# Performance work log

Measured on AMD Instinct MI355X. Metric: run time of the kernel, lower is better.

Reference implementation:

```python
import jax, jax.numpy as jnp
import numpy as np

N, IN_DIM, HID, LAT, E = 8192, 512, 256, 128, 262144


def gcn_conv(x, W, b, src, dst, n):
    # PyG-style GCNConv: linear transform, add self-loops, D^-1/2 A D^-1/2 aggregation, bias.
    h = x @ W                                                  # [n, out]
    loops = jnp.arange(n)
    s = jnp.concatenate([src, loops])
    d = jnp.concatenate([dst, loops])
    deg = jax.ops.segment_sum(jnp.ones(s.shape[0], x.dtype), d, num_segments=n)
    dinv = jnp.where(deg > 0, jax.lax.rsqrt(deg), jnp.zeros((), x.dtype))
    norm = dinv[s] * dinv[d]                                   # [E+n]
    out = jax.ops.segment_sum(h[s] * norm[:, None], d, num_segments=n)
    return out + b


def setup_inputs() -> dict:
    key = jax.random.key(0)
    ks = jax.random.split(key, 9)
    x = jax.random.normal(ks[0], (N, IN_DIM), dtype=jnp.float32)
    edge_index = jax.random.randint(ks[1], (2, E), 0, N, dtype=jnp.int64)
    eps = jax.random.normal(ks[2], (N, LAT), dtype=jnp.float32)
    # Glorot-ish scaled params
    W1 = jax.random.normal(ks[3], (IN_DIM, HID), dtype=jnp.float32) / np.sqrt(IN_DIM)
    b1 = jnp.zeros((HID,), jnp.float32)
    Wmu = jax.random.normal(ks[4], (HID, LAT), dtype=jnp.float32) / np.sqrt(HID)
    bmu = jnp.zeros((LAT,), jnp.float32)
    Wls = jax.random.normal(ks[5], (HID, LAT), dtype=jnp.float32) / np.sqrt(HID)
    bls = jnp.zeros((LAT,), jnp.float32)
    return {"x": x, "edge_index": edge_index, "eps": eps,
            "W1": W1, "b1": b1, "Wmu": Wmu, "bmu": bmu, "Wls": Wls, "bls": bls}


def reference(x, edge_index, eps, W1, b1, Wmu, bmu, Wls, bls):
    src, dst = edge_index[0], edge_index[1]
    n = x.shape[0]
    h = jax.nn.relu(gcn_conv(x, W1, b1, src, dst, n))          # [N, HID]
    mu = gcn_conv(h, Wmu, bmu, src, dst, n)                    # [N, LAT]
    logstd = gcn_conv(h, Wls, bls, src, dst, n)                # [N, LAT]
    z = eps * jnp.exp(logstd) + mu                             # reparametrize (training mode)
    adj_recon = jax.nn.sigmoid(z @ z.T)                        # [N, N]
    return adj_recon, mu, logstd
```

## Files before the change

kernel.cpp:

```cpp
#include <hip/hip_runtime.h>

#define N_NODES 8192
#define IN_DIM  512
#define HID     256
#define LAT     128
#define NEDGE   262144

typedef __attribute__((ext_vector_type(8))) short  bf16x8;
typedef __attribute__((ext_vector_type(4))) float  f32x4;
typedef unsigned short u16;
typedef __attribute__((ext_vector_type(4))) unsigned short u16x4;

static __device__ inline u16 f2bf(float f) {
    unsigned u = __float_as_uint(f);
    unsigned r = (u + 0x7fffu + ((u >> 16) & 1u)) >> 16;
    return (u16)r;
}
static __device__ inline float bf2f(u16 s) {
    return __uint_as_float(((unsigned)s) << 16);
}

#define PREP_BLOCKS 5888

static __device__ inline void convw_body(const float* __restrict__ W,
                                         u16* __restrict__ th,
                                         u16* __restrict__ tl,
                                         int K, int N, int Kld, int roff, int e) {
    if (e >= K * N) return;
    int k = e / N, n = e - k * N;
    float f = W[e];
    u16 hi = f2bf(f);
    u16 lo = f2bf(f - bf2f(hi));
    size_t o = (size_t)(roff + n) * Kld + k;
    th[o] = hi;
    tl[o] = lo;
}

__global__ __launch_bounds__(256) void prep_kernel(const int* __restrict__ dst,
                                                   int* __restrict__ cnt,
                                                   const float* __restrict__ X,
                                                   u16* __restrict__ xh,
                                                   u16* __restrict__ xl,
                                                   const float* __restrict__ W1,
                                                   u16* __restrict__ w1h,
                                                   u16* __restrict__ w1l,
                                                   const float* __restrict__ Wmu,
                                                   const float* __restrict__ Wls,
                                                   u16* __restrict__ wch,
                                                   u16* __restrict__ wcl) {
    const int b = blockIdx.x, t = threadIdx.x;
    if (b < 1024) {
        int e = b * 256 + t;
        atomicAdd(&cnt[dst[e]], 1);
    } else if (b < 5120) {
        int idx = (b - 1024) * 256 + t;
        f32x4 v = *(const f32x4*)(X + (size_t)idx * 4);
        u16x4 h, l;
#pragma unroll
        for (int j = 0; j < 4; ++j) {
            h[j] = f2bf(v[j]);
            l[j] = f2bf(v[j] - bf2f(h[j]));
        }
        *(u16x4*)(xh + (size_t)idx * 4) = h;
        *(u16x4*)(xl + (size_t)idx * 4) = l;
    } else if (b < 5632) {
        convw_body(W1, w1h, w1l, IN_DIM, HID, IN_DIM, 0, (b - 5120) * 256 + t);
    } else if (b < 5760) {
        convw_body(Wmu, wch, wcl, HID, LAT, HID, 0, (b - 5632) * 256 + t);
    } else {
        convw_body(Wls, wch, wcl, HID, LAT, HID, LAT, (b - 5760) * 256 + t);
    }
}

__global__ __launch_bounds__(256) void scan_kernel(const int* __restrict__ cnt,
                                                   int* __restrict__ rowptr,
                                                   int* __restrict__ cursor,
                                                   float* __restrict__ dinv) {
    __shared__ int part[256];
    const int t = threadIdx.x;
    const int base = t * 32;
    int local[32];
    int s = 0;
#pragma unroll
    for (int i = 0; i < 32; ++i) {
        int cv = cnt[base + i];
        local[i] = s; s += cv;
        dinv[base + i] = rsqrtf((float)cv + 1.0f);
    }
    part[t] = s;
    __syncthreads();
    for (int off = 1; off < 256; off <<= 1) {
        int v = 0;
        if (t >= off) v = part[t - off];
        __syncthreads();
        if (t >= off) part[t] += v;
        __syncthreads();
    }
    int pre = (t == 0) ? 0 : part[t - 1];
#pragma unroll
    for (int i = 0; i < 32; ++i) {
        int r = pre + local[i];
        rowptr[base + i] = r;
        cursor[base + i] = r;
    }
    if (t == 255) rowptr[8192] = part[255];
}

static __device__ inline void gemm_body(const u16* __restrict__ Ah,
                                        const u16* __restrict__ Al,
                                        const u16* __restrict__ Bth,
                                        const u16* __restrict__ Btl,
                                        float* __restrict__ C,
                                        int K, int ldc, int bx, int by, int tid) {
    const int lane = tid & 63;
    const int wave = tid >> 6;
    const int l16 = lane & 15, quad = lane >> 4;
    const int rowBase = by * 128 + (wave >> 1) * 64;
    const int colBase = bx * 128 + (wave & 1) * 64;

    f32x4 acc[4][4] = {};

    for (int k0 = 0; k0 < K; k0 += 32) {
        const int kk = k0 + quad * 8;
        bf16x8 ah[4], al[4], bh[4], bl[4];
#pragma unroll
        for (int r = 0; r < 4; ++r) {
            int row = rowBase + r * 16 + l16;
            ah[r] = *(const bf16x8*)(Ah + (size_t)row * K + kk);
            al[r] = *(const bf16x8*)(Al + (size_t)row * K + kk);
        }
#pragma unroll
        for (int c = 0; c < 4; ++c) {
            int row = colBase + c * 16 + l16;
            bh[c] = *(const bf16x8*)(Bth + (size_t)row * K + kk);
            bl[c] = *(const bf16x8*)(Btl + (size_t)row * K + kk);
        }
#pragma unroll
        for (int r = 0; r < 4; ++r)
#pragma unroll
            for (int c = 0; c < 4; ++c) {
                acc[r][c] = __builtin_amdgcn_mfma_f32_16x16x32_bf16(ah[r], bh[c], acc[r][c], 0, 0, 0);
                acc[r][c] = __builtin_amdgcn_mfma_f32_16x16x32_bf16(ah[r], bl[c], acc[r][c], 0, 0, 0);
                acc[r][c] = __builtin_amdgcn_mfma_f32_16x16x32_bf16(al[r], bh[c], acc[r][c], 0, 0, 0);
            }
    }

#pragma unroll
    for (int r = 0; r < 4; ++r)
#pragma unroll
        for (int c = 0; c < 4; ++c)
#pragma unroll
            for (int i = 0; i < 4; ++i) {
                int orow = rowBase + r * 16 + quad * 4 + i;
                int ocol = colBase + c * 16 + l16;
                C[(size_t)orow * ldc + ocol] = acc[r][c][i];
            }
}

__global__ __launch_bounds__(256) void fillgemm_kernel(const u16* __restrict__ xh,
                                                       const u16* __restrict__ xl,
                                                       const u16* __restrict__ w1h,
                                                       const u16* __restrict__ w1l,
                                                       float* __restrict__ pre1,
                                                       const int* __restrict__ src,
                                                       const int* __restrict__ dst,
                                                       int* __restrict__ cursor,
                                                       int* __restrict__ ebuf) {
    const int b = blockIdx.x;
    if (b < 128) {
        gemm_body(xh, xl, w1h, w1l, pre1, IN_DIM, HID, b & 1, b >> 1, threadIdx.x);
    } else {
        int e = (b - 128) * 256 + threadIdx.x;
        int pos = atomicAdd(&cursor[dst[e]], 1);
        ebuf[pos] = src[e];
    }
}

__global__ __launch_bounds__(256) void gemm2_kernel(const u16* __restrict__ h1h,
                                                    const u16* __restrict__ h1l,
                                                    const u16* __restrict__ wch,
                                                    const u16* __restrict__ wcl,
                                                    float* __restrict__ pre2) {
    gemm_body(h1h, h1l, wch, wcl, pre2, HID, HID, blockIdx.x & 1, blockIdx.x >> 1, threadIdx.x);
}

__global__ __launch_bounds__(256) void gather1_kernel(const float* __restrict__ pre1,
                                                      u16* __restrict__ h1h,
                                                      u16* __restrict__ h1l,
                                                      const int* __restrict__ rowptr,
                                                      const int* __restrict__ ebuf,
                                                      const float* __restrict__ dinv,
                                                      const float* __restrict__ b1) {
    const int wave = threadIdx.x >> 6, lane = threadIdx.x & 63;
    const int v = blockIdx.x * 4 + wave;
    const int c = lane * 4;
    const float dv = dinv[v];
    f32x4 acc = *(const f32x4*)(pre1 + (size_t)v * HID + c);
    acc *= dv * dv;
    int i = rowptr[v], end = rowptr[v + 1];
    for (; i + 1 < end; i += 2) {
        int s0 = ebuf[i], s1 = ebuf[i + 1];
        float n0 = dv * dinv[s0], n1 = dv * dinv[s1];
        f32x4 h0 = *(const f32x4*)(pre1 + (size_t)s0 * HID + c);
        f32x4 h1v = *(const f32x4*)(pre1 + (size_t)s1 * HID + c);
#pragma unroll
        for (int j = 0; j < 4; ++j) acc[j] += n0 * h0[j] + n1 * h1v[j];
    }
    if (i < end) {
        int s0 = ebuf[i];
        float n0 = dv * dinv[s0];
        f32x4 h0 = *(const f32x4*)(pre1 + (size_t)s0 * HID + c);
#pragma unroll
        for (int j = 0; j < 4; ++j) acc[j] += n0 * h0[j];
    }
    f32x4 bb = *(const f32x4*)(b1 + c);
    u16x4 hv, lv;
#pragma unroll
    for (int j = 0; j < 4; ++j) {
        float h = fmaxf(acc[j] + bb[j], 0.0f);
        hv[j] = f2bf(h);
        lv[j] = f2bf(h - bf2f(hv[j]));
    }
    *(u16x4*)(h1h + (size_t)v * HID + c) = hv;
    *(u16x4*)(h1l + (size_t)v * HID + c) = lv;
}

__global__ __launch_bounds__(256) void gather2_kernel(const float* __restrict__ pre2,
                                                      const int* __restrict__ rowptr,
                                                      const int* __restrict__ ebuf,
                                                      const float* __restrict__ dinv,
                                                      const float* __restrict__ bmu,
                                                      const float* __restrict__ bls,
                                                      const float* __restrict__ eps,
                                                      float* __restrict__ out_mu,
                                                      float* __restrict__ out_ls,
                                                      u16* __restrict__ zhi,
                                                      u16* __restrict__ zlo) {
    const int wave = threadIdx.x >> 6, lane = threadIdx.x & 63;
    const int v = blockIdx.x * 4 + wave;
    const int c = lane * 4;
    const float dv = dinv[v];
    f32x4 acc = *(const f32x4*)(pre2 + (size_t)v * HID + c);
    acc *= dv * dv;
    int i = rowptr[v], end = rowptr[v + 1];
    for (; i + 1 < end; i += 2) {
        int s0 = ebuf[i], s1 = ebuf[i + 1];
        float n0 = dv * dinv[s0], n1 = dv * dinv[s1];
        f32x4 h0 = *(const f32x4*)(pre2 + (size_t)s0 * HID + c);
        f32x4 h1v = *(const f32x4*)(pre2 + (size_t)s1 * HID + c);
#pragma unroll
        for (int j = 0; j < 4; ++j) acc[j] += n0 * h0[j] + n1 * h1v[j];
    }
    if (i < end) {
        int s0 = ebuf[i];
        float n0 = dv * dinv[s0];
        f32x4 h0 = *(const f32x4*)(pre2 + (size_t)s0 * HID + c);
#pragma unroll
        for (int j = 0; j < 4; ++j) acc[j] += n0 * h0[j];
    }
    const float* bias = (lane < 32) ? (bmu + c) : (bls + (c - 128));
    f32x4 bb = *(const f32x4*)bias;
#pragma unroll
    for (int j = 0; j < 4; ++j) acc[j] += bb[j];

    f32x4 other;
#pragma unroll
    for (int j = 0; j < 4; ++j) other[j] = __shfl(acc[j], (lane + 32) & 63, 64);

    if (lane < 32) {
        int idx = v * LAT + c;
        f32x4 ep = *(const f32x4*)(eps + idx);
        __builtin_nontemporal_store(acc, (f32x4*)(out_mu + idx));
        u16x4 hv, lv;
#pragma unroll
        for (int j = 0; j < 4; ++j) {
            float z = ep[j] * __expf(other[j]) + acc[j];
            u16 hi = f2bf(z);
            hv[j] = hi;
            lv[j] = f2bf(z - bf2f(hi));
        }
        *(u16x4*)(zhi + idx) = hv;
        *(u16x4*)(zlo + idx) = lv;
    } else {
        int idx = v * LAT + (c - 128);
        __builtin_nontemporal_store(acc, (f32x4*)(out_ls + idx));
    }
}

#define NTRI 2080
__global__ __launch_bounds__(256) void zzt_kernel(const u16* __restrict__ zhi,
                                                  const u16* __restrict__ zlo,
                                                  float* __restrict__ out) {
    __shared__ float lds[4][16][68];
    const int lane = threadIdx.x & 63;
    const int wave = threadIdx.x >> 6;
    const int l16 = lane & 15, quad = lane >> 4;

    int bid = (blockIdx.x & 7) * 260 + (blockIdx.x >> 3);
    int by = (int)((sqrtf(8.0f * (float)bid + 1.0f) - 1.0f) * 0.5f);
    while ((by + 1) * (by + 2) / 2 <= bid) ++by;
    while (by * (by + 1) / 2 > bid) --by;
    const int bx = bid - by * (by + 1) / 2;

    const int rowBase = by * 128 + (wave >> 1) * 64;
    const int colBase = bx * 128 + (wave & 1) * 64;

    f32x4 acc[4][4] = {};

#pragma unroll
    for (int k0 = 0; k0 < LAT; k0 += 32) {
        const int kk = k0 + quad * 8;
        bf16x8 ah[4], al[4], bh[4], bl[4];
#pragma unroll
        for (int r = 0; r < 4; ++r) {
            int row = rowBase + r * 16 + l16;
            ah[r] = *(const bf16x8*)(zhi + (size_t)row * LAT + kk);
            al[r] = *(const bf16x8*)(zlo + (size_t)row * LAT + kk);
        }
#pragma unroll
        for (int c = 0; c < 4; ++c) {
            int row = colBase + c * 16 + l16;
            bh[c] = *(const bf16x8*)(zhi + (size_t)row * LAT + kk);
            bl[c] = *(const bf16x8*)(zlo + (size_t)row * LAT + kk);
        }
#pragma unroll
        for (int r = 0; r < 4; ++r)
#pragma unroll
            for (int c = 0; c < 4; ++c) {
                acc[r][c] = __builtin_amdgcn_mfma_f32_16x16x32_bf16(ah[r], bh[c], acc[r][c], 0, 0, 0);
                acc[r][c] = __builtin_amdgcn_mfma_f32_16x16x32_bf16(ah[r], bl[c], acc[r][c], 0, 0, 0);
                acc[r][c] = __builtin_amdgcn_mfma_f32_16x16x32_bf16(al[r], bh[c], acc[r][c], 0, 0, 0);
            }
    }

#pragma unroll
    for (int r = 0; r < 4; ++r)
#pragma unroll
        for (int c = 0; c < 4; ++c)
#pragma unroll
            for (int i = 0; i < 4; ++i)
                acc[r][c][i] = 1.0f / (1.0f + __expf(-acc[r][c][i]));

#pragma unroll
    for (int r = 0; r < 4; ++r) {
#pragma unroll
        for (int c = 0; c < 4; ++c)
#pragma unroll
            for (int i = 0; i < 4; ++i)
                lds[wave][quad * 4 + i][c * 16 + l16] = acc[r][c][i];
#pragma unroll
        for (int it = 0; it < 4; ++it) {
            f32x4 v = *(const f32x4*)&lds[wave][it * 4 + quad][l16 * 4];
            int orow = rowBase + r * 16 + it * 4 + quad;
            __builtin_nontemporal_store(v, (f32x4*)(out + (size_t)orow * N_NODES + colBase + l16 * 4));
        }
    }

    if (by != bx) {
#pragma unroll
        for (int c = 0; c < 4; ++c) {
#pragma unroll
            for (int r = 0; r < 4; ++r) {
                f32x4 tv = acc[r][c];
                *(f32x4*)&lds[wave][l16][r * 16 + quad * 4] = tv;
            }
#pragma unroll
            for (int it = 0; it < 4; ++it) {
                f32x4 v = *(const f32x4*)&lds[wave][it * 4 + quad][l16 * 4];
                int orow = colBase + c * 16 + it * 4 + quad;
                __builtin_nontemporal_store(v, (f32x4*)(out + (size_t)orow * N_NODES + rowBase + l16 * 4));
            }
        }
    }
}

extern "C" void kernel_launch(void* const* d_in, const int* in_sizes, int n_in,
                              void* d_out, int out_size, void* d_ws, size_t ws_size,
                              hipStream_t stream) {
    const float* x   = (const float*)d_in[0];
    const int*   ei  = (const int*)d_in[1];
    const float* eps = (const float*)d_in[2];
    const float* W1  = (const float*)d_in[3];
    const float* b1  = (const float*)d_in[4];
    const float* Wmu = (const float*)d_in[5];
    const float* bmu = (const float*)d_in[6];
    const float* Wls = (const float*)d_in[7];
    const float* bls = (const float*)d_in[8];
    const int* src = ei;
    const int* dst = ei + NEDGE;

    float* out = (float*)d_out;
    float* pre1 = out;
    float* pre2 = out + 2097152;
    int*   ibase  = (int*)(out + 4194304);
    int*   cnt    = ibase;
    int*   rowptr = ibase + 8192;
    int*   cursor = ibase + 16385;
    int*   ebuf   = ibase + 24577;
    u16* xhi    = (u16*)(out + 4587520);
    u16* xlo    = (u16*)(out + 6684672);
    u16* h1hi   = (u16*)(out + 8781824);
    u16* h1lo   = (u16*)(out + 9830400);
    u16* w1thi  = (u16*)(out + 10878976);
    u16* w1tlo  = (u16*)(out + 11010048);
    u16* wcathi = (u16*)(out + 11141120);
    u16* wcatlo = (u16*)(out + 11173888);
    float* out_mu = out + 67108864;
    float* out_ls = out + 68157440;

    float* dinv = (float*)d_ws;
    u16* zhi = (u16*)((char*)d_ws + 32768);
    u16* zlo = (u16*)((char*)d_ws + 32768 + 2097152);

    hipMemsetAsync(cnt, 0, 8192 * sizeof(int), stream);

    prep_kernel<<<PREP_BLOCKS, 256, 0, stream>>>(dst, cnt, x, xhi, xlo,
                                                 W1, w1thi, w1tlo, Wmu, Wls, wcathi, wcatlo);

    scan_kernel<<<1, 256, 0, stream>>>(cnt, rowptr, cursor, dinv);

    fillgemm_kernel<<<128 + 1024, 256, 0, stream>>>(xhi, xlo, w1thi, w1tlo, pre1,
                                                    src, dst, cursor, ebuf);

    gather1_kernel<<<N_NODES / 4, 256, 0, stream>>>(pre1, h1hi, h1lo, rowptr, ebuf, dinv, b1);

    gemm2_kernel<<<128, 256, 0, stream>>>(h1hi, h1lo, wcathi, wcatlo, pre2);

    gather2_kernel<<<N_NODES / 4, 256, 0, stream>>>(pre2, rowptr, ebuf, dinv, bmu, bls, eps,
                                                    out_mu, out_ls, zhi, zlo);

    zzt_kernel<<<NTRI, 256, 0, stream>>>(zhi, zlo, out);
}
```

Before: 495.5 us.

## Switch zzt to 32x32x16 MFMA and unroll gathers by four edges

The z·zᵀ kernel now uses 32x32x16 bf16 MFMA tiles (2x2 per wave) instead of 16x16x32 (4x4). Operands are swapped so that row-contiguous accumulator values can be staged through a larger LDS buffer for the direct and transposed stores. Both gather kernels add a 4-edge unrolled loop so more independent neighbor loads are in flight. The aim is to cut operand load instructions in the GEMM and raise memory-level parallelism in the gathers, at the cost of more LDS use and a more complex store remap.

```diff
diff --git a/kernel.cpp b/kernel.cpp
--- a/kernel.cpp
+++ b/kernel.cpp
@@ -6,8 +6,9 @@
 #define LAT     128
 #define NEDGE   262144
 
-typedef __attribute__((ext_vector_type(8))) short  bf16x8;
-typedef __attribute__((ext_vector_type(4))) float  f32x4;
+typedef __attribute__((ext_vector_type(8)))  short  bf16x8;
+typedef __attribute__((ext_vector_type(4)))  float  f32x4;
+typedef __attribute__((ext_vector_type(16))) float  f32x16;
 typedef unsigned short u16;
 typedef __attribute__((ext_vector_type(4))) unsigned short u16x4;
 
@@ -198,6 +199,18 @@
     f32x4 acc = *(const f32x4*)(pre1 + (size_t)v * HID + c);
     acc *= dv * dv;
     int i = rowptr[v], end = rowptr[v + 1];
+    for (; i + 3 < end; i += 4) {
+        int s0 = ebuf[i], s1 = ebuf[i + 1], s2 = ebuf[i + 2], s3 = ebuf[i + 3];
+        float n0 = dv * dinv[s0], n1 = dv * dinv[s1];
+        float n2 = dv * dinv[s2], n3 = dv * dinv[s3];
+        f32x4 h0 = *(const f32x4*)(pre1 + (size_t)s0 * HID + c);
+        f32x4 h1v = *(const f32x4*)(pre1 + (size_t)s1 * HID + c);
+        f32x4 h2 = *(const f32x4*)(pre1 + (size_t)s2 * HID + c);
+        f32x4 h3 = *(const f32x4*)(pre1 + (size_t)s3 * HID + c);
+#pragma unroll
+        for (int j = 0; j < 4; ++j)
+            acc[j] += (n0 * h0[j] + n1 * h1v[j]) + (n2 * h2[j] + n3 * h3[j]);
+    }
     for (; i + 1 < end; i += 2) {
         int s0 = ebuf[i], s1 = ebuf[i + 1];
         float n0 = dv * dinv[s0], n1 = dv * dinv[s1];
@@ -243,6 +256,18 @@
     f32x4 acc = *(const f32x4*)(pre2 + (size_t)v * HID + c);
     acc *= dv * dv;
     int i = rowptr[v], end = rowptr[v + 1];
+    for (; i + 3 < end; i += 4) {
+        int s0 = ebuf[i], s1 = ebuf[i + 1], s2 = ebuf[i + 2], s3 = ebuf[i + 3];
+        float n0 = dv * dinv[s0], n1 = dv * dinv[s1];
+        float n2 = dv * dinv[s2], n3 = dv * dinv[s3];
+        f32x4 h0 = *(const f32x4*)(pre2 + (size_t)s0 * HID + c);
+        f32x4 h1v = *(const f32x4*)(pre2 + (size_t)s1 * HID + c);
+        f32x4 h2 = *(const f32x4*)(pre2 + (size_t)s2 * HID + c);
+        f32x4 h3 = *(const f32x4*)(pre2 + (size_t)s3 * HID + c);
+#pragma unroll
+        for (int j = 0; j < 4; ++j)
+            acc[j] += (n0 * h0[j] + n1 * h1v[j]) + (n2 * h2[j] + n3 * h3[j]);
+    }
     for (; i + 1 < end; i += 2) {
         int s0 = ebuf[i], s1 = ebuf[i + 1];
         float n0 = dv * dinv[s0], n1 = dv * dinv[s1];
@@ -291,10 +316,11 @@
 __global__ __launch_bounds__(256) void zzt_kernel(const u16* __restrict__ zhi,
                                                   const u16* __restrict__ zlo,
                                                   float* __restrict__ out) {
-    __shared__ float lds[4][16][68];
+    __shared__ float lds[4][32][68];
     const int lane = threadIdx.x & 63;
     const int wave = threadIdx.x >> 6;
     const int l16 = lane & 15, quad = lane >> 4;
+    const int l32 = lane & 31, half = lane >> 5;
 
     int bid = (blockIdx.x & 7) * 260 + (blockIdx.x >> 3);
     int by = (int)((sqrtf(8.0f * (float)bid + 1.0f) - 1.0f) * 0.5f);
@@ -305,69 +331,74 @@
     const int rowBase = by * 128 + (wave >> 1) * 64;
     const int colBase = bx * 128 + (wave & 1) * 64;
 
-    f32x4 acc[4][4] = {};
-
-#pragma unroll
-    for (int k0 = 0; k0 < LAT; k0 += 32) {
-        const int kk = k0 + quad * 8;
-        bf16x8 ah[4], al[4], bh[4], bl[4];
-#pragma unroll
-        for (int r = 0; r < 4; ++r) {
-            int row = rowBase + r * 16 + l16;
-            ah[r] = *(const bf16x8*)(zhi + (size_t)row * LAT + kk);
-            al[r] = *(const bf16x8*)(zlo + (size_t)row * LAT + kk);
-        }
-#pragma unroll
-        for (int c = 0; c < 4; ++c) {
-            int row = colBase + c * 16 + l16;
-            bh[c] = *(const bf16x8*)(zhi + (size_t)row * LAT + kk);
-            bl[c] = *(const bf16x8*)(zlo + (size_t)row * LAT + kk);
-        }
-#pragma unroll
-        for (int r = 0; r < 4; ++r)
-#pragma unroll
-            for (int c = 0; c < 4; ++c) {
-                acc[r][c] = __builtin_amdgcn_mfma_f32_16x16x32_bf16(ah[r], bh[c], acc[r][c], 0, 0, 0);
-                acc[r][c] = __builtin_amdgcn_mfma_f32_16x16x32_bf16(ah[r], bl[c], acc[r][c], 0, 0, 0);
-                acc[r][c] = __builtin_amdgcn_mfma_f32_16x16x32_bf16(al[r], bh[c], acc[r][c], 0, 0, 0);
+    f32x16 acc[2][2] = {};
+
+#pragma unroll
+    for (int k = 0; k < 8; ++k) {
+        const int kk = k * 16 + half * 8;
+        bf16x8 xh[2], xl[2], yh[2], yl[2];
+#pragma unroll
+        for (int r = 0; r < 2; ++r) {
+            int row = rowBase + r * 32 + l32;
+            xh[r] = *(const bf16x8*)(zhi + (size_t)row * LAT + kk);
+            xl[r] = *(const bf16x8*)(zlo + (size_t)row * LAT + kk);
+        }
+#pragma unroll
+        for (int cc = 0; cc < 2; ++cc) {
+            int row = colBase + cc * 32 + l32;
+            yh[cc] = *(const bf16x8*)(zhi + (size_t)row * LAT + kk);
+            yl[cc] = *(const bf16x8*)(zlo + (size_t)row * LAT + kk);
+        }
+#pragma unroll
+        for (int r = 0; r < 2; ++r)
+#pragma unroll
+            for (int cc = 0; cc < 2; ++cc) {
+                acc[r][cc] = __builtin_amdgcn_mfma_f32_32x32x16_bf16(yh[cc], xh[r], acc[r][cc], 0, 0, 0);
+                acc[r][cc] = __builtin_amdgcn_mfma_f32_32x32x16_bf16(yh[cc], xl[r], acc[r][cc], 0, 0, 0);
+                acc[r][cc] = __builtin_amdgcn_mfma_f32_32x32x16_bf16(yl[cc], xh[r], acc[r][cc], 0, 0, 0);
             }
     }
 
 #pragma unroll
-    for (int r = 0; r < 4; ++r)
-#pragma unroll
-        for (int c = 0; c < 4; ++c)
-#pragma unroll
-            for (int i = 0; i < 4; ++i)
-                acc[r][c][i] = 1.0f / (1.0f + __expf(-acc[r][c][i]));
-
-#pragma unroll
-    for (int r = 0; r < 4; ++r) {
-#pragma unroll
-        for (int c = 0; c < 4; ++c)
-#pragma unroll
-            for (int i = 0; i < 4; ++i)
-                lds[wave][quad * 4 + i][c * 16 + l16] = acc[r][c][i];
-#pragma unroll
-        for (int it = 0; it < 4; ++it) {
+    for (int r = 0; r < 2; ++r)
+#pragma unroll
+        for (int cc = 0; cc < 2; ++cc)
+#pragma unroll
+            for (int i = 0; i < 16; ++i)
+                acc[r][cc][i] = 1.0f / (1.0f + __expf(-acc[r][cc][i]));
+
+#pragma unroll
+    for (int r = 0; r < 2; ++r) {
+#pragma unroll
+        for (int cc = 0; cc < 2; ++cc)
+#pragma unroll
+            for (int q = 0; q < 4; ++q) {
+                f32x4 v = { acc[r][cc][q * 4 + 0], acc[r][cc][q * 4 + 1],
+                            acc[r][cc][q * 4 + 2], acc[r][cc][q * 4 + 3] };
+                *(f32x4*)&lds[wave][l32][cc * 32 + q * 8 + half * 4] = v;
+            }
+#pragma unroll
+        for (int it = 0; it < 8; ++it) {
             f32x4 v = *(const f32x4*)&lds[wave][it * 4 + quad][l16 * 4];
-            int orow = rowBase + r * 16 + it * 4 + quad;
+            int orow = rowBase + r * 32 + it * 4 + quad;
             __builtin_nontemporal_store(v, (f32x4*)(out + (size_t)orow * N_NODES + colBase + l16 * 4));
         }
     }
 
     if (by != bx) {
 #pragma unroll
-        for (int c = 0; c < 4; ++c) {
-#pragma unroll
-            for (int r = 0; r < 4; ++r) {
-                f32x4 tv = acc[r][c];
-                *(f32x4*)&lds[wave][l16][r * 16 + quad * 4] = tv;
-            }
-#pragma unroll
-            for (int it = 0; it < 4; ++it) {
+        for (int cc = 0; cc < 2; ++cc) {
+#pragma unroll
+            for (int r = 0; r < 2; ++r)
+#pragma unroll
+                for (int q = 0; q < 4; ++q)
+#pragma unroll
+                    for (int t = 0; t < 4; ++t)
+                        lds[wave][q * 8 + half * 4 + t][r * 32 + l32] = acc[r][cc][q * 4 + t];
+#pragma unroll
+            for (int it = 0; it < 8; ++it) {
                 f32x4 v = *(const f32x4*)&lds[wave][it * 4 + quad][l16 * 4];
-                int orow = colBase + c * 16 + it * 4 + quad;
+                int orow = colBase + cc * 32 + it * 4 + quad;
                 __builtin_nontemporal_store(v, (f32x4*)(out + (size_t)orow * N_NODES + rowBase + l16 * 4));
             }
         }
```

Result: faster. 475.4 us (-4.1%).
